# Performance work log

Measured on AMD Instinct MI355X. Metric: run time of the kernel, lower is better.

The kernel has to match this reference:

```python
import jax, jax.numpy as jnp
import numpy as np

B, N, DIM = 4, 1024, 768
H, GP = 12, 64
HD = DIM // H
SCALE = HD ** -0.5


def setup_inputs() -> dict:
    key = jax.random.key(0)
    ks = jax.random.split(key, 7)
    s = DIM ** -0.5
    return {
        "x": jax.random.normal(ks[0], (B, N, DIM), dtype=jnp.float32),
        "W_qkv": jax.random.normal(ks[1], (3 * DIM, DIM), dtype=jnp.float32) * s,
        "b_qkv": jnp.zeros((3 * DIM,), dtype=jnp.float32),
        "W_gp": jax.random.normal(ks[2], (GP, DIM), dtype=jnp.float32) * s,
        "alpha": jax.random.normal(ks[3], (1, H, 1, 1), dtype=jnp.float32),
        "W_proj": jax.random.normal(ks[4], (DIM, DIM), dtype=jnp.float32) * s,
        "b_proj": jnp.zeros((DIM,), dtype=jnp.float32),
    }


def reference(x, W_qkv, b_qkv, W_gp, alpha, W_proj, b_proj):
    b, n, c = x.shape
    # qkv projection, split into heads: [b, h, n, hd]
    qkv = x @ W_qkv.T + b_qkv
    q, k, v = jnp.split(qkv, 3, axis=-1)
    def to_heads(t):
        return t.reshape(b, n, H, HD).transpose(0, 2, 1, 3)
    q, k, v = to_heads(q), to_heads(k), to_heads(v)

    # raw attention scores [b, h, n, n]
    attn = jnp.einsum('bhnd,bhmd->bhnm', q, k) * SCALE

    # group similarity: gp weight viewed as [h, gp, hd]
    gp = W_gp.reshape(H, GP, HD)
    gw = jnp.einsum('bhnd,hmd->bhnm', v, gp)          # [b, h, n, gp]
    gw = jax.nn.gelu(gw, approximate=False)           # exact GELU (torch default)
    gw = jax.nn.softmax(gw, axis=-1)
    G = jnp.einsum('bhnm,bhkm->bhnk', gw, gw)         # [b, h, n, n]

    # gated combination
    attn = jax.nn.softmax(attn * G, axis=-1)
    a = jax.nn.sigmoid(alpha)                          # [1, h, 1, 1]
    A = (1.0 - a) * attn + a * G
    # column-sum renormalization (sum over query dim 2)
    A = A / (A.sum(axis=2, keepdims=True) + 1e-8)

    out = jnp.einsum('bhnm,bhmd->bhnd', A, v)
    out = out.transpose(0, 2, 1, 3).reshape(b, n, c)
    return out @ W_proj.T + b_proj
```

## Files before the change

kernel.cpp:

```cpp
#include <hip/hip_runtime.h>
#include <math.h>

namespace {

constexpr int kN   = 1024;
constexpr int kDim = 768;
constexpr int kH   = 12;
constexpr int kBH  = 48;
constexpr float kScale = 0.125f;

typedef __attribute__((ext_vector_type(8))) short short8;
typedef __attribute__((ext_vector_type(4))) short short4v;
typedef __attribute__((ext_vector_type(4))) float f32x4;
typedef __attribute__((ext_vector_type(16))) float f32x16;
typedef __attribute__((ext_vector_type(4))) uint uint4v;

#define MFMA(a, b, c)   __builtin_amdgcn_mfma_f32_16x16x32_bf16(a, b, c, 0, 0, 0)
#define MFMA32(a, b, c) __builtin_amdgcn_mfma_f32_32x32x16_bf16(a, b, c, 0, 0, 0)

__device__ __forceinline__ ushort f2bf(float f) {
  uint u = __builtin_bit_cast(uint, f);
  u += 0x7fffu + ((u >> 16) & 1u);
  return (ushort)(u >> 16);
}
__device__ __forceinline__ float bf2f(ushort h) {
  uint u = ((uint)h) << 16;
  return __builtin_bit_cast(float, u);
}
__device__ __forceinline__ void split8(const float* f, short8& hi, short8& lo) {
  #pragma unroll
  for (int i = 0; i < 8; i++) {
    const ushort h = f2bf(f[i]);
    hi[i] = (short)h;
    lo[i] = (short)f2bf(f[i] - bf2f(h));
  }
}
__device__ __forceinline__ uint packbf(float a, float b) {
  return (uint)f2bf(a) | ((uint)f2bf(b) << 16);
}

__device__ __forceinline__ void gl16(const short* g, short* l) {
  __builtin_amdgcn_global_load_lds(
      (const __attribute__((address_space(1))) void*)g,
      (__attribute__((address_space(3))) void*)l, 16, 0, 0);
}

__device__ __forceinline__ short8 frag(const short* t, int row, int chunk) {
  return *(const short8*)(t + row * 64 + ((chunk ^ (row & 7)) << 3));
}

template<int ROWS, int W>
__device__ __forceinline__ void stage_tile(short* dst, const short* src,
                                           int stride, int w, int l) {
  #pragma unroll
  for (int c = 0; c < ROWS / 8; c += W) {
    const int cc = c + w;
    const int row0 = cc << 3;
    const int row = row0 + (l >> 3);
    const int ch = (l & 7) ^ (row & 7);
    gl16(src + (size_t)row * stride + (ch << 3), dst + row0 * 64);
  }
}

__global__ __launch_bounds__(256) void k_split(const float* __restrict__ src,
                                               short* __restrict__ h,
                                               short* __restrict__ l) {
  const size_t i = ((size_t)blockIdx.x * 256 + threadIdx.x) * 4;
  const float4 f = *(const float4*)(src + i);
  const float ff[4] = {f.x, f.y, f.z, f.w};
  short4v hv, lv;
  #pragma unroll
  for (int j = 0; j < 4; j++) {
    const ushort u = f2bf(ff[j]);
    hv[j] = (short)u;
    lv[j] = (short)f2bf(ff[j] - bf2f(u));
  }
  *(short4v*)(h + i) = hv;
  *(short4v*)(l + i) = lv;
}

__global__ __launch_bounds__(512) void k_qkv(const short* __restrict__ xh,
                                             const short* __restrict__ xl,
                                             const short* __restrict__ wh,
                                             const short* __restrict__ wl,
                                             const float* __restrict__ bias,
                                             short* __restrict__ qh, short* __restrict__ ql,
                                             short* __restrict__ kh, short* __restrict__ kl,
                                             short* __restrict__ vh, short* __restrict__ vl) {
  __shared__ __align__(16) short sb[2][32768];
  const int bx = blockIdx.x, by = blockIdx.y;
  const int tid = threadIdx.x, w = tid >> 6, lane = tid & 63;
  const int wr = w >> 2, wc = w & 3;
  const short* Asrc_h = xh + (size_t)(by * 128) * kDim;
  const short* Asrc_l = xl + (size_t)(by * 128) * kDim;
  const short* Bsrc_h = wh + (size_t)(bx * 128) * kDim;
  const short* Bsrc_l = wl + (size_t)(bx * 128) * kDim;

  f32x4 acc[4][2] = {};
  {
    short* nb = sb[0];
    stage_tile<128, 8>(nb,          Asrc_h, kDim, w, lane);
    stage_tile<128, 8>(nb + 8192,   Asrc_l, kDim, w, lane);
    stage_tile<128, 8>(nb + 16384,  Bsrc_h, kDim, w, lane);
    stage_tile<128, 8>(nb + 24576,  Bsrc_l, kDim, w, lane);
  }
  int p = 0;
  #pragma unroll 1
  for (int t = 0; t < 12; ++t) {
    __syncthreads();
    if (t < 11) {
      const int k0 = (t + 1) * 64;
      short* nb = sb[p ^ 1];
      stage_tile<128, 8>(nb,         Asrc_h + k0, kDim, w, lane);
      stage_tile<128, 8>(nb + 8192,  Asrc_l + k0, kDim, w, lane);
      stage_tile<128, 8>(nb + 16384, Bsrc_h + k0, kDim, w, lane);
      stage_tile<128, 8>(nb + 24576, Bsrc_l + k0, kDim, w, lane);
    }
    const short* cb = sb[p];
    #pragma unroll
    for (int s = 0; s < 2; ++s) {
      const int ch = (s << 2) + (lane >> 4);
      short8 af[4], alf[4], bf_[2], blf[2];
      #pragma unroll
      for (int i = 0; i < 4; i++) {
        const int ar = wr * 64 + i * 16 + (lane & 15);
        af[i]  = frag(cb, ar, ch);
        alf[i] = frag(cb + 8192, ar, ch);
      }
      #pragma unroll
      for (int j = 0; j < 2; j++) {
        const int br = wc * 32 + j * 16 + (lane & 15);
        bf_[j] = frag(cb + 16384, br, ch);
        blf[j] = frag(cb + 24576, br, ch);
      }
      #pragma unroll
      for (int i = 0; i < 4; i++)
        #pragma unroll
        for (int j = 0; j < 2; j++) {
          acc[i][j] = MFMA(af[i], bf_[j], acc[i][j]);
          acc[i][j] = MFMA(af[i], blf[j], acc[i][j]);
          acc[i][j] = MFMA(alf[i], bf_[j], acc[i][j]);
        }
    }
    p ^= 1;
  }
  #pragma unroll
  for (int j = 0; j < 2; j++) {
    const int col = bx * 128 + wc * 32 + j * 16 + (lane & 15);
    const int part = col / 768;
    const int rem = col - part * 768;
    const int hh = rem >> 6, d = rem & 63;
    short* dh = (part == 0) ? qh : ((part == 1) ? kh : vh);
    short* dl = (part == 0) ? ql : ((part == 1) ? kl : vl);
    const float bv = bias[col];
    #pragma unroll
    for (int i = 0; i < 4; i++) {
      #pragma unroll
      for (int r = 0; r < 4; r++) {
        const int gr = by * 128 + wr * 64 + i * 16 + ((lane >> 4) << 2) + r;
        const int b = gr >> 10, n = gr & 1023;
        const float val = acc[i][j][r] + bv;
        const ushort hu = f2bf(val);
        const size_t idx = (size_t)((b * kH + hh) * kN + n) * 64 + d;
        dh[idx] = (short)hu;
        dl[idx] = (short)f2bf(val - bf2f(hu));
      }
    }
  }
}

__global__ __launch_bounds__(512) void k_gw(const short* __restrict__ vh,
                                            const short* __restrict__ vl,
                                            const float* __restrict__ Wgp,
                                            short* __restrict__ gwh,
                                            short* __restrict__ gwl) {
  const int bh = blockIdx.x;
  const int h = bh % kH;
  const int n0 = blockIdx.y << 7;
  const int tid = threadIdx.x, w = tid >> 6, lane = tid & 63;
  __shared__ __align__(16) short gph[4096], gpl[4096];
  {
    const int r = tid >> 3, c = tid & 7;
    float f[8] __attribute__((aligned(16)));
    *(float4*)(f + 0) = *(const float4*)(Wgp + h * 4096 + r * 64 + c * 8);
    *(float4*)(f + 4) = *(const float4*)(Wgp + h * 4096 + r * 64 + c * 8 + 4);
    short8 hh, ll;
    split8(f, hh, ll);
    const int slot = c ^ (r & 7);
    *(short8*)(gph + r * 64 + slot * 8) = hh;
    *(short8*)(gpl + r * 64 + slot * 8) = ll;
  }
  short8 vhf[2], vlf[2];
  const size_t arow = (size_t)(bh * kN + n0 + w * 16 + (lane & 15)) * 64 + ((lane >> 4) << 3);
  vhf[0] = *(const short8*)(vh + arow); vhf[1] = *(const short8*)(vh + arow + 32);
  vlf[0] = *(const short8*)(vl + arow); vlf[1] = *(const short8*)(vl + arow + 32);
  __syncthreads();

  f32x4 aU[4] = {};
  #pragma unroll
  for (int msub = 0; msub < 4; msub++) {
    #pragma unroll
    for (int s = 0; s < 2; s++) {
      const int row = (msub << 4) + (lane & 15);
      const int ch = (s << 2) + (lane >> 4);
      const short8 bh_ = frag(gph, row, ch);
      const short8 bl_ = frag(gpl, row, ch);
      aU[msub] = MFMA(vhf[s], bh_, aU[msub]);
      aU[msub] = MFMA(vhf[s], bl_, aU[msub]);
      aU[msub] = MFMA(vlf[s], bh_, aU[msub]);
    }
  }
  #pragma unroll
  for (int r = 0; r < 4; r++) {
    float u[4];
    #pragma unroll
    for (int m = 0; m < 4; m++) {
      const float a = aU[m][r];
      u[m] = 0.5f * a * (1.0f + erff(a * 0.70710678118654752f));
    }
    float mx = fmaxf(fmaxf(u[0], u[1]), fmaxf(u[2], u[3]));
    #pragma unroll
    for (int msk = 1; msk < 16; msk <<= 1) mx = fmaxf(mx, __shfl_xor(mx, msk));
    float e[4], ssum = 0.f;
    #pragma unroll
    for (int m = 0; m < 4; m++) { e[m] = __expf(u[m] - mx); ssum += e[m]; }
    #pragma unroll
    for (int msk = 1; msk < 16; msk <<= 1) ssum += __shfl_xor(ssum, msk);
    const float inv = 1.0f / ssum;
    const int n = n0 + w * 16 + ((lane >> 4) << 2) + r;
    #pragma unroll
    for (int m = 0; m < 4; m++) {
      const float g = e[m] * inv;
      const ushort hu = f2bf(g);
      const size_t idx = (size_t)(bh * kN + n) * 64 + (m << 4) + (lane & 15);
      gwh[idx] = (short)hu;
      gwl[idx] = (short)f2bf(g - bf2f(hu));
    }
  }
}

__global__ __launch_bounds__(256) void k_vt(const short* __restrict__ vh,
                                            const float* __restrict__ rcolv,
                                            short* __restrict__ vtg) {
  const int bh = blockIdx.x;
  const int n0 = blockIdx.y << 6;
  __shared__ short t[64][80];
  const int tid = threadIdx.x;
  {
    const int n = tid >> 2, d0 = (tid & 3) << 4;
    const float rc = rcolv[bh * kN + n0 + n];
    const short8 a = *(const short8*)(vh + (size_t)(bh * kN + n0 + n) * 64 + d0);
    const short8 b = *(const short8*)(vh + (size_t)(bh * kN + n0 + n) * 64 + d0 + 8);
    #pragma unroll
    for (int i = 0; i < 8; ++i) {
      t[d0 + i][n]     = (short)f2bf(bf2f((ushort)a[i]) * rc);
      t[d0 + 8 + i][n] = (short)f2bf(bf2f((ushort)b[i]) * rc);
    }
  }
  __syncthreads();
  const int d = tid >> 2, j0 = (tid & 3) << 4;
  short* dst = vtg + (size_t)bh * 65536 + (size_t)d * 1024 + n0 + j0;
  *(short8*)(dst)     = *(const short8*)(&t[d][j0]);
  *(short8*)(dst + 8) = *(const short8*)(&t[d][j0 + 8]);
}

__global__ __launch_bounds__(256) void k_denom(const short* __restrict__ qh,
                                               const short* __restrict__ ql,
                                               const short* __restrict__ kh,
                                               const short* __restrict__ kl,
                                               const short* __restrict__ gwh,
                                               const short* __restrict__ gwl,
                                               float* __restrict__ rdenom) {
  const int bh = blockIdx.x;
  const int n0 = blockIdx.y << 7;
  const int tid = threadIdx.x, w = tid >> 6, lane = tid & 63;
  const int lc = lane & 31, hl = lane >> 5;
  __shared__ __align__(16) short sb[16384];

  short8 qB[4], qlB[4], gB[4], glB[4];
  {
    const size_t nrow = (size_t)(bh * kN + n0 + w * 32 + lc) * 64;
    #pragma unroll
    for (int ks = 0; ks < 4; ks++) {
      const int off = ks * 16 + (hl << 3);
      qB[ks]  = *(const short8*)(qh  + nrow + off);
      qlB[ks] = *(const short8*)(ql  + nrow + off);
      gB[ks]  = *(const short8*)(gwh + nrow + off);
      glB[ks] = *(const short8*)(gwl + nrow + off);
    }
  }
  float dsum = 0.f;
  #pragma unroll 1
  for (int t = 0; t < 16; ++t) {
    __syncthreads();
    const size_t mo = (size_t)(bh * kN + t * 64) * 64;
    stage_tile<64, 4>(sb,         kh  + mo, 64, w, lane);
    stage_tile<64, 4>(sb + 4096,  kl  + mo, 64, w, lane);
    stage_tile<64, 4>(sb + 8192,  gwh + mo, 64, w, lane);
    stage_tile<64, 4>(sb + 12288, gwl + mo, 64, w, lane);
    __syncthreads();
    #pragma unroll
    for (int at = 0; at < 2; ++at) {
      f32x16 aS = {}, aG = {};
      #pragma unroll
      for (int ks = 0; ks < 4; ++ks) {
        const int row = at * 32 + lc;
        const int ck = ks * 2 + hl;
        const short8 Ah_ = frag(sb, row, ck);
        const short8 Al_ = frag(sb + 4096, row, ck);
        const short8 Eh_ = frag(sb + 8192, row, ck);
        const short8 El_ = frag(sb + 12288, row, ck);
        aS = MFMA32(Ah_, qB[ks], aS);
        aS = MFMA32(Al_, qB[ks], aS);
        aS = MFMA32(Ah_, qlB[ks], aS);
        aG = MFMA32(Eh_, gB[ks], aG);
        aG = MFMA32(El_, gB[ks], aG);
        aG = MFMA32(Eh_, glB[ks], aG);
      }
      #pragma unroll
      for (int r = 0; r < 16; ++r)
        dsum += __expf(aS[r] * kScale * aG[r]);
    }
  }
  dsum += __shfl_xor(dsum, 32);
  if (lane < 32) rdenom[bh * kN + n0 + w * 32 + lane] = 1.0f / dsum;
}

__global__ __launch_bounds__(256) void k_colsum(const short* __restrict__ qh,
                                                const short* __restrict__ ql,
                                                const short* __restrict__ kh,
                                                const short* __restrict__ kl,
                                                const short* __restrict__ gwh,
                                                const short* __restrict__ gwl,
                                                const float* __restrict__ rdenom,
                                                const float* __restrict__ alpha,
                                                float* __restrict__ rcolv) {
  const int bh = blockIdx.x;
  const int m0 = blockIdx.y << 7;
  const int tid = threadIdx.x, w = tid >> 6, lane = tid & 63;
  const int lc = lane & 31, hl = lane >> 5;
  __shared__ __align__(16) short sb[16384];
  __shared__ float rdl[64];
  const float ah_ = 1.0f / (1.0f + __expf(-alpha[bh % kH]));
  const float om = 1.0f - ah_;

  short8 kB[4], klB[4], gB[4], glB[4];
  {
    const size_t mrow = (size_t)(bh * kN + m0 + w * 32 + lc) * 64;
    #pragma unroll
    for (int ks = 0; ks < 4; ks++) {
      const int off = ks * 16 + (hl << 3);
      kB[ks]  = *(const short8*)(kh  + mrow + off);
      klB[ks] = *(const short8*)(kl  + mrow + off);
      gB[ks]  = *(const short8*)(gwh + mrow + off);
      glB[ks] = *(const short8*)(gwl + mrow + off);
    }
  }
  float csum = 0.f;
  #pragma unroll 1
  for (int t = 0; t < 16; ++t) {
    __syncthreads();
    const size_t no = (size_t)(bh * kN + t * 64) * 64;
    stage_tile<64, 4>(sb,         qh  + no, 64, w, lane);
    stage_tile<64, 4>(sb + 4096,  ql  + no, 64, w, lane);
    stage_tile<64, 4>(sb + 8192,  gwh + no, 64, w, lane);
    stage_tile<64, 4>(sb + 12288, gwl + no, 64, w, lane);
    if (tid < 64) rdl[tid] = rdenom[bh * kN + t * 64 + tid];
    __syncthreads();
    #pragma unroll
    for (int at = 0; at < 2; ++at) {
      f32x16 aS = {}, aG = {};
      #pragma unroll
      for (int ks = 0; ks < 4; ++ks) {
        const int row = at * 32 + lc;
        const int ck = ks * 2 + hl;
        const short8 Ah_ = frag(sb, row, ck);
        const short8 Al_ = frag(sb + 4096, row, ck);
        const short8 Eh_ = frag(sb + 8192, row, ck);
        const short8 El_ = frag(sb + 12288, row, ck);
        aS = MFMA32(Ah_, kB[ks], aS);
        aS = MFMA32(Al_, kB[ks], aS);
        aS = MFMA32(Ah_, klB[ks], aS);
        aG = MFMA32(Eh_, gB[ks], aG);
        aG = MFMA32(El_, gB[ks], aG);
        aG = MFMA32(Eh_, glB[ks], aG);
      }
      #pragma unroll
      for (int r = 0; r < 16; ++r) {
        const int nr = at * 32 + (r & 3) + ((r >> 2) << 3) + (hl << 2);
        const float g = aG[r];
        csum += om * (__expf(aS[r] * kScale * g) * rdl[nr]) + ah_ * g;
      }
    }
  }
  csum += __shfl_xor(csum, 32);
  if (lane < 32) rcolv[bh * kN + m0 + w * 32 + lane] = 1.0f / (csum + 1e-8f);
}

__global__ __launch_bounds__(256) void k_out(const short* __restrict__ qh,
                                             const short* __restrict__ ql,
                                             const short* __restrict__ kh,
                                             const short* __restrict__ kl,
                                             const short* __restrict__ vtg,
                                             const short* __restrict__ gwh,
                                             const short* __restrict__ gwl,
                                             const float* __restrict__ rdenom,
                                             const float* __restrict__ alpha,
                                             short* __restrict__ ctxh,
                                             short* __restrict__ ctxl) {
  const int bh = blockIdx.x;
  const int h = bh % kH;
  const int b = bh / kH;
  const int n0 = blockIdx.y << 7;
  const int tid = threadIdx.x, w = tid >> 6, lane = tid & 63;
  const int lc = lane & 31, hl = lane >> 5;
  __shared__ __align__(16) short sb[20480];
  const float ah_ = 1.0f / (1.0f + __expf(-alpha[h]));
  const float om = 1.0f - ah_;

  short8 qB[4], qlB[4], gB[4], glB[4];
  {
    const size_t nrow = (size_t)(bh * kN + n0 + w * 32 + lc) * 64;
    #pragma unroll
    for (int ks = 0; ks < 4; ks++) {
      const int off = ks * 16 + (hl << 3);
      qB[ks]  = *(const short8*)(qh  + nrow + off);
      qlB[ks] = *(const short8*)(ql  + nrow + off);
      gB[ks]  = *(const short8*)(gwh + nrow + off);
      glB[ks] = *(const short8*)(gwl + nrow + off);
    }
  }
  const float rdn = rdenom[bh * kN + n0 + w * 32 + lc];
  f32x16 oac[2] = {};

  #pragma unroll 1
  for (int t = 0; t < 16; ++t) {
    __syncthreads();
    const size_t mo = (size_t)(bh * kN + t * 64) * 64;
    stage_tile<64, 4>(sb,         kh  + mo, 64, w, lane);
    stage_tile<64, 4>(sb + 4096,  kl  + mo, 64, w, lane);
    stage_tile<64, 4>(sb + 8192,  gwh + mo, 64, w, lane);
    stage_tile<64, 4>(sb + 12288, gwl + mo, 64, w, lane);
    stage_tile<64, 4>(sb + 16384, vtg + (size_t)bh * 65536 + t * 64, kN, w, lane);
    __syncthreads();
    short8 pf[4];
    #pragma unroll
    for (int at = 0; at < 2; ++at) {
      f32x16 aS = {}, aG = {};
      #pragma unroll
      for (int ks = 0; ks < 4; ++ks) {
        const int row = at * 32 + lc;
        const int ck = ks * 2 + hl;
        const short8 Ah_ = frag(sb, row, ck);
        const short8 Al_ = frag(sb + 4096, row, ck);
        const short8 Eh_ = frag(sb + 8192, row, ck);
        const short8 El_ = frag(sb + 12288, row, ck);
        aS = MFMA32(Ah_, qB[ks], aS);
        aS = MFMA32(Al_, qB[ks], aS);
        aS = MFMA32(Ah_, qlB[ks], aS);
        aG = MFMA32(Eh_, gB[ks], aG);
        aG = MFMA32(El_, gB[ks], aG);
        aG = MFMA32(Eh_, glB[ks], aG);
      }
      float a[16];
      #pragma unroll
      for (int r = 0; r < 16; ++r) {
        const float g = aG[r];
        const float p = __expf(aS[r] * kScale * g) * rdn;
        a[r] = om * p + ah_ * g;
      }
      uint W[8], Ws[8];
      #pragma unroll
      for (int j = 0; j < 8; ++j) W[j] = packbf(a[2 * j], a[2 * j + 1]);
      #pragma unroll
      for (int j = 0; j < 8; ++j) Ws[j] = __shfl_xor(W[j], 32);
      {
        uint4v b0, b1;
        b0[0] = hl ? Ws[2] : W[0];  b0[1] = hl ? Ws[3] : W[1];
        b0[2] = hl ? W[2]  : Ws[0]; b0[3] = hl ? W[3]  : Ws[1];
        b1[0] = hl ? Ws[6] : W[4];  b1[1] = hl ? Ws[7] : W[5];
        b1[2] = hl ? W[6]  : Ws[4]; b1[3] = hl ? W[7]  : Ws[5];
        pf[at * 2 + 0] = __builtin_bit_cast(short8, b0);
        pf[at * 2 + 1] = __builtin_bit_cast(short8, b1);
      }
    }
    #pragma unroll
    for (int dt = 0; dt < 2; ++dt)
      #pragma unroll
      for (int ks = 0; ks < 4; ++ks) {
        const short8 va = frag(sb + 16384, dt * 32 + lc, ks * 2 + hl);
        oac[dt] = MFMA32(va, pf[ks], oac[dt]);
      }
  }
  __syncthreads();
  float* ow = (float*)sb;
  const int wbase = w * 32 * 68;
  #pragma unroll
  for (int dt = 0; dt < 2; ++dt)
    #pragma unroll
    for (int r = 0; r < 16; ++r) {
      const int d = dt * 32 + (r & 3) + ((r >> 2) << 3) + (hl << 2);
      ow[wbase + lc * 68 + d] = oac[dt][r];
    }
  __syncthreads();
  {
    const int rowi = tid >> 1;
    const int d0 = (tid & 1) << 5;
    const float* src = ow + (rowi >> 5) * 32 * 68 + (rowi & 31) * 68 + d0;
    float f[32] __attribute__((aligned(16)));
    #pragma unroll
    for (int j = 0; j < 8; ++j) *(float4*)(f + 4 * j) = *(const float4*)(src + 4 * j);
    const int n = n0 + rowi;
    short* dsth = ctxh + (size_t)(b * kN + n) * kDim + h * 64 + d0;
    short* dstl = ctxl + (size_t)(b * kN + n) * kDim + h * 64 + d0;
    #pragma unroll
    for (int g8 = 0; g8 < 4; ++g8) {
      short8 hi, lo;
      split8(f + 8 * g8, hi, lo);
      *(short8*)(dsth + 8 * g8) = hi;
      *(short8*)(dstl + 8 * g8) = lo;
    }
  }
}

__global__ __launch_bounds__(512) void k_proj(const short* __restrict__ ch_,
                                              const short* __restrict__ cl_,
                                              const short* __restrict__ wh,
                                              const short* __restrict__ wl,
                                              const float* __restrict__ bias,
                                              float* __restrict__ out) {
  __shared__ __align__(16) short sb[2][32768];
  const int bx = blockIdx.x, by = blockIdx.y;
  const int tid = threadIdx.x, w = tid >> 6, lane = tid & 63;
  const int wr = w >> 2, wc = w & 3;
  const short* Asrc_h = ch_ + (size_t)(by * 128) * kDim;
  const short* Asrc_l = cl_ + (size_t)(by * 128) * kDim;
  const short* Bsrc_h = wh + (size_t)(bx * 128) * kDim;
  const short* Bsrc_l = wl + (size_t)(bx * 128) * kDim;

  f32x4 acc[4][2] = {};
  {
    short* nb = sb[0];
    stage_tile<128, 8>(nb,         Asrc_h, kDim, w, lane);
    stage_tile<128, 8>(nb + 8192,  Asrc_l, kDim, w, lane);
    stage_tile<128, 8>(nb + 16384, Bsrc_h, kDim, w, lane);
    stage_tile<128, 8>(nb + 24576, Bsrc_l, kDim, w, lane);
  }
  int p = 0;
  #pragma unroll 1
  for (int t = 0; t < 12; ++t) {
    __syncthreads();
    if (t < 11) {
      const int k0 = (t + 1) * 64;
      short* nb = sb[p ^ 1];
      stage_tile<128, 8>(nb,         Asrc_h + k0, kDim, w, lane);
      stage_tile<128, 8>(nb + 8192,  Asrc_l + k0, kDim, w, lane);
      stage_tile<128, 8>(nb + 16384, Bsrc_h + k0, kDim, w, lane);
      stage_tile<128, 8>(nb + 24576, Bsrc_l + k0, kDim, w, lane);
    }
    const short* cb = sb[p];
    #pragma unroll
    for (int s = 0; s < 2; ++s) {
      const int ch = (s << 2) + (lane >> 4);
      short8 af[4], alf[4], bf_[2], blf[2];
      #pragma unroll
      for (int i = 0; i < 4; i++) {
        const int ar = wr * 64 + i * 16 + (lane & 15);
        af[i]  = frag(cb, ar, ch);
        alf[i] = frag(cb + 8192, ar, ch);
      }
      #pragma unroll
      for (int j = 0; j < 2; j++) {
        const int br = wc * 32 + j * 16 + (lane & 15);
        bf_[j] = frag(cb + 16384, br, ch);
        blf[j] = frag(cb + 24576, br, ch);
      }
      #pragma unroll
      for (int i = 0; i < 4; i++)
        #pragma unroll
        for (int j = 0; j < 2; j++) {
          acc[i][j] = MFMA(af[i], bf_[j], acc[i][j]);
          acc[i][j] = MFMA(af[i], blf[j], acc[i][j]);
          acc[i][j] = MFMA(alf[i], bf_[j], acc[i][j]);
          acc[i][j] = MFMA(alf[i], blf[j], acc[i][j]);
        }
    }
    p ^= 1;
  }
  #pragma unroll
  for (int j = 0; j < 2; j++) {
    const int col = bx * 128 + wc * 32 + j * 16 + (lane & 15);
    const float bv = bias[col];
    #pragma unroll
    for (int i = 0; i < 4; i++) {
      #pragma unroll
      for (int r = 0; r < 4; r++) {
        const int row = by * 128 + wr * 64 + i * 16 + ((lane >> 4) << 2) + r;
        out[(size_t)row * kDim + col] = acc[i][j][r] + bv;
      }
    }
  }
}

}

extern "C" void kernel_launch(void* const* d_in, const int* in_sizes, int n_in,
                              void* d_out, int out_size, void* d_ws, size_t ws_size,
                              hipStream_t stream) {
  const float* x     = (const float*)d_in[0];
  const float* Wqkv  = (const float*)d_in[1];
  const float* bqkv  = (const float*)d_in[2];
  const float* Wgp   = (const float*)d_in[3];
  const float* alpha = (const float*)d_in[4];
  const float* Wproj = (const float*)d_in[5];
  const float* bproj = (const float*)d_in[6];
  float* out = (float*)d_out;

  const size_t he = 3145728;
  short* qh  = (short*)d_ws;
  short* ql  = qh + he;
  short* kh  = ql + he;
  short* kl  = kh + he;
  short* vh  = kl + he;
  short* vl  = vh + he;
  short* gwh = vl + he;
  short* gwl = gwh + he;
  short* xh  = gwl + he;
  short* xl  = xh + he;
  float* rdenom = (float*)(xl + he);
  float* rcolv  = rdenom + (size_t)kBH * kN;

  short* Wqh = gwh;  short* Wql = gwl;
  short* vtg = vl;
  short* ctxh = xh;  short* ctxl = xl;
  short* Wph = qh;   short* Wpl = ql;

  k_split<<<3072, 256, 0, stream>>>(x, xh, xl);
  k_split<<<1728, 256, 0, stream>>>(Wqkv, Wqh, Wql);
  k_qkv  <<<dim3(18, 32), 512, 0, stream>>>(xh, xl, Wqh, Wql, bqkv,
                                            qh, ql, kh, kl, vh, vl);
  k_gw   <<<dim3(kBH, 8), 512, 0, stream>>>(vh, vl, Wgp, gwh, gwl);
  k_denom<<<dim3(kBH, 8), 256, 0, stream>>>(qh, ql, kh, kl, gwh, gwl, rdenom);
  k_colsum<<<dim3(kBH, 8), 256, 0, stream>>>(qh, ql, kh, kl, gwh, gwl,
                                             rdenom, alpha, rcolv);
  k_vt   <<<dim3(kBH, 16), 256, 0, stream>>>(vh, rcolv, vtg);
  k_out  <<<dim3(kBH, 8), 256, 0, stream>>>(qh, ql, kh, kl, vtg, gwh, gwl,
                                            rdenom, alpha, ctxh, ctxl);
  k_split<<<576, 256, 0, stream>>>(Wproj, Wph, Wpl);
  k_proj <<<dim3(6, 32), 512, 0, stream>>>(ctxh, ctxl, Wph, Wpl, bproj, out);
}
```

Baseline: 274.2 us.

## Split key dimension across wave groups in attention kernels and fold scale into q

```diff
diff --git a/kernel.cpp b/kernel.cpp
--- a/kernel.cpp
+++ b/kernel.cpp
@@ -153,13 +153,14 @@
     short* dh = (part == 0) ? qh : ((part == 1) ? kh : vh);
     short* dl = (part == 0) ? ql : ((part == 1) ? kl : vl);
     const float bv = bias[col];
+    const float scl = (part == 0) ? kScale : 1.0f;
     #pragma unroll
     for (int i = 0; i < 4; i++) {
       #pragma unroll
       for (int r = 0; r < 4; r++) {
         const int gr = by * 128 + wr * 64 + i * 16 + ((lane >> 4) << 2) + r;
         const int b = gr >> 10, n = gr & 1023;
-        const float val = acc[i][j][r] + bv;
+        const float val = (acc[i][j][r] + bv) * scl;
         const ushort hu = f2bf(val);
         const size_t idx = (size_t)((b * kH + hh) * kN + n) * 64 + d;
         dh[idx] = (short)hu;
@@ -264,22 +265,25 @@
   *(short8*)(dst + 8) = *(const short8*)(&t[d][j0 + 8]);
 }
 
-__global__ __launch_bounds__(256) void k_denom(const short* __restrict__ qh,
-                                               const short* __restrict__ ql,
-                                               const short* __restrict__ kh,
-                                               const short* __restrict__ kl,
-                                               const short* __restrict__ gwh,
-                                               const short* __restrict__ gwl,
-                                               float* __restrict__ rdenom) {
+__global__ __launch_bounds__(256, 3) void k_denom(const short* __restrict__ qh,
+                                                  const short* __restrict__ ql,
+                                                  const short* __restrict__ kh,
+                                                  const short* __restrict__ kl,
+                                                  const short* __restrict__ gwh,
+                                                  const short* __restrict__ gwl,
+                                                  float* __restrict__ rdenom) {
   const int bh = blockIdx.x;
-  const int n0 = blockIdx.y << 7;
+  const int n0 = blockIdx.y << 6;
   const int tid = threadIdx.x, w = tid >> 6, lane = tid & 63;
   const int lc = lane & 31, hl = lane >> 5;
-  __shared__ __align__(16) short sb[16384];
+  const int nw = w & 1, mh = w >> 1;
+  __shared__ __align__(16) short sb[32768];
+  __shared__ float part[4][32];
+  const short* my = sb + mh * 16384;
 
   short8 qB[4], qlB[4], gB[4], glB[4];
   {
-    const size_t nrow = (size_t)(bh * kN + n0 + w * 32 + lc) * 64;
+    const size_t nrow = (size_t)(bh * kN + n0 + nw * 32 + lc) * 64;
     #pragma unroll
     for (int ks = 0; ks < 4; ks++) {
       const int off = ks * 16 + (hl << 3);
@@ -291,13 +295,18 @@
   }
   float dsum = 0.f;
   #pragma unroll 1
-  for (int t = 0; t < 16; ++t) {
-    __syncthreads();
-    const size_t mo = (size_t)(bh * kN + t * 64) * 64;
-    stage_tile<64, 4>(sb,         kh  + mo, 64, w, lane);
-    stage_tile<64, 4>(sb + 4096,  kl  + mo, 64, w, lane);
-    stage_tile<64, 4>(sb + 8192,  gwh + mo, 64, w, lane);
-    stage_tile<64, 4>(sb + 12288, gwl + mo, 64, w, lane);
+  for (int t = 0; t < 8; ++t) {
+    __syncthreads();
+    const size_t mo0 = (size_t)(bh * kN + t * 64) * 64;
+    const size_t mo1 = (size_t)(bh * kN + 512 + t * 64) * 64;
+    stage_tile<64, 4>(sb,          kh  + mo0, 64, w, lane);
+    stage_tile<64, 4>(sb + 4096,   kl  + mo0, 64, w, lane);
+    stage_tile<64, 4>(sb + 8192,   gwh + mo0, 64, w, lane);
+    stage_tile<64, 4>(sb + 12288,  gwl + mo0, 64, w, lane);
+    stage_tile<64, 4>(sb + 16384,  kh  + mo1, 64, w, lane);
+    stage_tile<64, 4>(sb + 20480,  kl  + mo1, 64, w, lane);
+    stage_tile<64, 4>(sb + 24576,  gwh + mo1, 64, w, lane);
+    stage_tile<64, 4>(sb + 28672,  gwl + mo1, 64, w, lane);
     __syncthreads();
     #pragma unroll
     for (int at = 0; at < 2; ++at) {
@@ -306,10 +315,10 @@
       for (int ks = 0; ks < 4; ++ks) {
         const int row = at * 32 + lc;
         const int ck = ks * 2 + hl;
-        const short8 Ah_ = frag(sb, row, ck);
-        const short8 Al_ = frag(sb + 4096, row, ck);
-        const short8 Eh_ = frag(sb + 8192, row, ck);
-        const short8 El_ = frag(sb + 12288, row, ck);
+        const short8 Ah_ = frag(my, row, ck);
+        const short8 Al_ = frag(my + 4096, row, ck);
+        const short8 Eh_ = frag(my + 8192, row, ck);
+        const short8 El_ = frag(my + 12288, row, ck);
         aS = MFMA32(Ah_, qB[ks], aS);
         aS = MFMA32(Al_, qB[ks], aS);
         aS = MFMA32(Ah_, qlB[ks], aS);
@@ -319,34 +328,41 @@
       }
       #pragma unroll
       for (int r = 0; r < 16; ++r)
-        dsum += __expf(aS[r] * kScale * aG[r]);
+        dsum += __expf(aS[r] * aG[r]);
     }
   }
   dsum += __shfl_xor(dsum, 32);
-  if (lane < 32) rdenom[bh * kN + n0 + w * 32 + lane] = 1.0f / dsum;
-}
-
-__global__ __launch_bounds__(256) void k_colsum(const short* __restrict__ qh,
-                                                const short* __restrict__ ql,
-                                                const short* __restrict__ kh,
-                                                const short* __restrict__ kl,
-                                                const short* __restrict__ gwh,
-                                                const short* __restrict__ gwl,
-                                                const float* __restrict__ rdenom,
-                                                const float* __restrict__ alpha,
-                                                float* __restrict__ rcolv) {
+  if (hl == 0) part[w][lc] = dsum;
+  __syncthreads();
+  if (tid < 64)
+    rdenom[bh * kN + n0 + tid] =
+        1.0f / (part[tid >> 5][tid & 31] + part[2 + (tid >> 5)][tid & 31]);
+}
+
+__global__ __launch_bounds__(256, 3) void k_colsum(const short* __restrict__ qh,
+                                                   const short* __restrict__ ql,
+                                                   const short* __restrict__ kh,
+                                                   const short* __restrict__ kl,
+                                                   const short* __restrict__ gwh,
+                                                   const short* __restrict__ gwl,
+                                                   const float* __restrict__ rdenom,
+                                                   const float* __restrict__ alpha,
+                                                   float* __restrict__ rcolv) {
   const int bh = blockIdx.x;
-  const int m0 = blockIdx.y << 7;
+  const int m0 = blockIdx.y << 6;
   const int tid = threadIdx.x, w = tid >> 6, lane = tid & 63;
   const int lc = lane & 31, hl = lane >> 5;
-  __shared__ __align__(16) short sb[16384];
-  __shared__ float rdl[64];
+  const int mw = w & 1, nh = w >> 1;
+  __shared__ __align__(16) short sb[32768];
+  __shared__ float part[4][32];
+  __shared__ float rdl[2][64];
+  const short* my = sb + nh * 16384;
   const float ah_ = 1.0f / (1.0f + __expf(-alpha[bh % kH]));
   const float om = 1.0f - ah_;
 
   short8 kB[4], klB[4], gB[4], glB[4];
   {
-    const size_t mrow = (size_t)(bh * kN + m0 + w * 32 + lc) * 64;
+    const size_t mrow = (size_t)(bh * kN + m0 + mw * 32 + lc) * 64;
     #pragma unroll
     for (int ks = 0; ks < 4; ks++) {
       const int off = ks * 16 + (hl << 3);
@@ -358,14 +374,21 @@
   }
   float csum = 0.f;
   #pragma unroll 1
-  for (int t = 0; t < 16; ++t) {
-    __syncthreads();
-    const size_t no = (size_t)(bh * kN + t * 64) * 64;
-    stage_tile<64, 4>(sb,         qh  + no, 64, w, lane);
-    stage_tile<64, 4>(sb + 4096,  ql  + no, 64, w, lane);
-    stage_tile<64, 4>(sb + 8192,  gwh + no, 64, w, lane);
-    stage_tile<64, 4>(sb + 12288, gwl + no, 64, w, lane);
-    if (tid < 64) rdl[tid] = rdenom[bh * kN + t * 64 + tid];
+  for (int t = 0; t < 8; ++t) {
+    __syncthreads();
+    const size_t no0 = (size_t)(bh * kN + t * 64) * 64;
+    const size_t no1 = (size_t)(bh * kN + 512 + t * 64) * 64;
+    stage_tile<64, 4>(sb,          qh  + no0, 64, w, lane);
+    stage_tile<64, 4>(sb + 4096,   ql  + no0, 64, w, lane);
+    stage_tile<64, 4>(sb + 8192,   gwh + no0, 64, w, lane);
+    stage_tile<64, 4>(sb + 12288,  gwl + no0, 64, w, lane);
+    stage_tile<64, 4>(sb + 16384,  qh  + no1, 64, w, lane);
+    stage_tile<64, 4>(sb + 20480,  ql  + no1, 64, w, lane);
+    stage_tile<64, 4>(sb + 24576,  gwh + no1, 64, w, lane);
+    stage_tile<64, 4>(sb + 28672,  gwl + no1, 64, w, lane);
+    if (tid < 128)
+      rdl[tid >> 6][tid & 63] =
+          rdenom[bh * kN + (tid >> 6) * 512 + t * 64 + (tid & 63)];
     __syncthreads();
     #pragma unroll
     for (int at = 0; at < 2; ++at) {
@@ -374,10 +397,10 @@
       for (int ks = 0; ks < 4; ++ks) {
         const int row = at * 32 + lc;
         const int ck = ks * 2 + hl;
-        const short8 Ah_ = frag(sb, row, ck);
-        const short8 Al_ = frag(sb + 4096, row, ck);
-        const short8 Eh_ = frag(sb + 8192, row, ck);
-        const short8 El_ = frag(sb + 12288, row, ck);
+        const short8 Ah_ = frag(my, row, ck);
+        const short8 Al_ = frag(my + 4096, row, ck);
+        const short8 Eh_ = frag(my + 8192, row, ck);
+        const short8 El_ = frag(my + 12288, row, ck);
         aS = MFMA32(Ah_, kB[ks], aS);
         aS = MFMA32(Al_, kB[ks], aS);
         aS = MFMA32(Ah_, klB[ks], aS);
@@ -389,38 +412,44 @@
       for (int r = 0; r < 16; ++r) {
         const int nr = at * 32 + (r & 3) + ((r >> 2) << 3) + (hl << 2);
         const float g = aG[r];
-        csum += om * (__expf(aS[r] * kScale * g) * rdl[nr]) + ah_ * g;
+        csum += om * (__expf(aS[r] * g) * rdl[nh][nr]) + ah_ * g;
       }
     }
   }
   csum += __shfl_xor(csum, 32);
-  if (lane < 32) rcolv[bh * kN + m0 + w * 32 + lane] = 1.0f / (csum + 1e-8f);
-}
-
-__global__ __launch_bounds__(256) void k_out(const short* __restrict__ qh,
-                                             const short* __restrict__ ql,
-                                             const short* __restrict__ kh,
-                                             const short* __restrict__ kl,
-                                             const short* __restrict__ vtg,
-                                             const short* __restrict__ gwh,
-                                             const short* __restrict__ gwl,
-                                             const float* __restrict__ rdenom,
-                                             const float* __restrict__ alpha,
-                                             short* __restrict__ ctxh,
-                                             short* __restrict__ ctxl) {
+  if (hl == 0) part[w][lc] = csum;
+  __syncthreads();
+  if (tid < 64)
+    rcolv[bh * kN + m0 + tid] =
+        1.0f / (part[tid >> 5][tid & 31] + part[2 + (tid >> 5)][tid & 31] + 1e-8f);
+}
+
+__global__ __launch_bounds__(512, 4) void k_out(const short* __restrict__ qh,
+                                                const short* __restrict__ ql,
+                                                const short* __restrict__ kh,
+                                                const short* __restrict__ kl,
+                                                const short* __restrict__ vtg,
+                                                const short* __restrict__ gwh,
+                                                const short* __restrict__ gwl,
+                                                const float* __restrict__ rdenom,
+                                                const float* __restrict__ alpha,
+                                                short* __restrict__ ctxh,
+                                                short* __restrict__ ctxl) {
   const int bh = blockIdx.x;
   const int h = bh % kH;
   const int b = bh / kH;
   const int n0 = blockIdx.y << 7;
   const int tid = threadIdx.x, w = tid >> 6, lane = tid & 63;
   const int lc = lane & 31, hl = lane >> 5;
-  __shared__ __align__(16) short sb[20480];
+  const int nw = w & 3, mh = w >> 2;
+  __shared__ __align__(16) short sb[40960];
   const float ah_ = 1.0f / (1.0f + __expf(-alpha[h]));
   const float om = 1.0f - ah_;
+  const short* my = sb + mh * 20480;
 
   short8 qB[4], qlB[4], gB[4], glB[4];
   {
-    const size_t nrow = (size_t)(bh * kN + n0 + w * 32 + lc) * 64;
+    const size_t nrow = (size_t)(bh * kN + n0 + nw * 32 + lc) * 64;
     #pragma unroll
     for (int ks = 0; ks < 4; ks++) {
       const int off = ks * 16 + (hl << 3);
@@ -430,18 +459,24 @@
       glB[ks] = *(const short8*)(gwl + nrow + off);
     }
   }
-  const float rdn = rdenom[bh * kN + n0 + w * 32 + lc];
+  const float rdn = rdenom[bh * kN + n0 + nw * 32 + lc];
   f32x16 oac[2] = {};
 
   #pragma unroll 1
-  for (int t = 0; t < 16; ++t) {
-    __syncthreads();
-    const size_t mo = (size_t)(bh * kN + t * 64) * 64;
-    stage_tile<64, 4>(sb,         kh  + mo, 64, w, lane);
-    stage_tile<64, 4>(sb + 4096,  kl  + mo, 64, w, lane);
-    stage_tile<64, 4>(sb + 8192,  gwh + mo, 64, w, lane);
-    stage_tile<64, 4>(sb + 12288, gwl + mo, 64, w, lane);
-    stage_tile<64, 4>(sb + 16384, vtg + (size_t)bh * 65536 + t * 64, kN, w, lane);
+  for (int t = 0; t < 8; ++t) {
+    __syncthreads();
+    const size_t mo0 = (size_t)(bh * kN + t * 64) * 64;
+    const size_t mo1 = (size_t)(bh * kN + 512 + t * 64) * 64;
+    stage_tile<64, 8>(sb,          kh  + mo0, 64, w, lane);
+    stage_tile<64, 8>(sb + 4096,   kl  + mo0, 64, w, lane);
+    stage_tile<64, 8>(sb + 8192,   gwh + mo0, 64, w, lane);
+    stage_tile<64, 8>(sb + 12288,  gwl + mo0, 64, w, lane);
+    stage_tile<64, 8>(sb + 16384,  vtg + (size_t)bh * 65536 + t * 64, kN, w, lane);
+    stage_tile<64, 8>(sb + 20480,  kh  + mo1, 64, w, lane);
+    stage_tile<64, 8>(sb + 24576,  kl  + mo1, 64, w, lane);
+    stage_tile<64, 8>(sb + 28672,  gwh + mo1, 64, w, lane);
+    stage_tile<64, 8>(sb + 32768,  gwl + mo1, 64, w, lane);
+    stage_tile<64, 8>(sb + 36864,  vtg + (size_t)bh * 65536 + 512 + t * 64, kN, w, lane);
     __syncthreads();
     short8 pf[4];
     #pragma unroll
@@ -451,10 +486,10 @@
       for (int ks = 0; ks < 4; ++ks) {
         const int row = at * 32 + lc;
         const int ck = ks * 2 + hl;
-        const short8 Ah_ = frag(sb, row, ck);
-        const short8 Al_ = frag(sb + 4096, row, ck);
-        const short8 Eh_ = frag(sb + 8192, row, ck);
-        const short8 El_ = frag(sb + 12288, row, ck);
+        const short8 Ah_ = frag(my, row, ck);
+        const short8 Al_ = frag(my + 4096, row, ck);
+        const short8 Eh_ = frag(my + 8192, row, ck);
+        const short8 El_ = frag(my + 12288, row, ck);
         aS = MFMA32(Ah_, qB[ks], aS);
         aS = MFMA32(Al_, qB[ks], aS);
         aS = MFMA32(Ah_, qlB[ks], aS);
@@ -466,7 +501,7 @@
       #pragma unroll
       for (int r = 0; r < 16; ++r) {
         const float g = aG[r];
-        const float p = __expf(aS[r] * kScale * g) * rdn;
+        const float p = __expf(aS[r] * g) * rdn;
         a[r] = om * p + ah_ * g;
       }
       uint W[8], Ws[8];
@@ -488,33 +523,45 @@
     for (int dt = 0; dt < 2; ++dt)
       #pragma unroll
       for (int ks = 0; ks < 4; ++ks) {
-        const short8 va = frag(sb + 16384, dt * 32 + lc, ks * 2 + hl);
+        const short8 va = frag(my + 16384, dt * 32 + lc, ks * 2 + hl);
         oac[dt] = MFMA32(va, pf[ks], oac[dt]);
       }
   }
   __syncthreads();
-  float* ow = (float*)sb;
-  const int wbase = w * 32 * 68;
-  #pragma unroll
-  for (int dt = 0; dt < 2; ++dt)
-    #pragma unroll
-    for (int r = 0; r < 16; ++r) {
-      const int d = dt * 32 + (r & 3) + ((r >> 2) << 3) + (hl << 2);
-      ow[wbase + lc * 68 + d] = oac[dt][r];
-    }
+  float* buf = (float*)sb;
+  if (mh == 1) {
+    #pragma unroll
+    for (int dt = 0; dt < 2; ++dt)
+      #pragma unroll
+      for (int r = 0; r < 16; ++r) {
+        const int d = dt * 32 + (r & 3) + ((r >> 2) << 3) + (hl << 2);
+        buf[(nw * 32 + lc) * 68 + d] = oac[dt][r];
+      }
+  }
   __syncthreads();
-  {
-    const int rowi = tid >> 1;
-    const int d0 = (tid & 1) << 5;
-    const float* src = ow + (rowi >> 5) * 32 * 68 + (rowi & 31) * 68 + d0;
-    float f[32] __attribute__((aligned(16)));
-    #pragma unroll
-    for (int j = 0; j < 8; ++j) *(float4*)(f + 4 * j) = *(const float4*)(src + 4 * j);
+  if (mh == 0) {
+    #pragma unroll
+    for (int dt = 0; dt < 2; ++dt)
+      #pragma unroll
+      for (int r = 0; r < 16; ++r) {
+        const int d = dt * 32 + (r & 3) + ((r >> 2) << 3) + (hl << 2);
+        const int idx = (nw * 32 + lc) * 68 + d;
+        buf[idx] = oac[dt][r] + buf[idx];
+      }
+  }
+  __syncthreads();
+  {
+    const int rowi = tid >> 2;
+    const int d0 = (tid & 3) << 4;
+    float f[16] __attribute__((aligned(16)));
+    #pragma unroll
+    for (int j = 0; j < 4; ++j)
+      *(float4*)(f + 4 * j) = *(const float4*)(&buf[rowi * 68 + d0 + 4 * j]);
     const int n = n0 + rowi;
     short* dsth = ctxh + (size_t)(b * kN + n) * kDim + h * 64 + d0;
     short* dstl = ctxl + (size_t)(b * kN + n) * kDim + h * 64 + d0;
     #pragma unroll
-    for (int g8 = 0; g8 < 4; ++g8) {
+    for (int g8 = 0; g8 < 2; ++g8) {
       short8 hi, lo;
       split8(f + 8 * g8, hi, lo);
       *(short8*)(dsth + 8 * g8) = hi;
@@ -640,11 +687,11 @@
   k_qkv  <<<dim3(18, 32), 512, 0, stream>>>(xh, xl, Wqh, Wql, bqkv,
                                             qh, ql, kh, kl, vh, vl);
   k_gw   <<<dim3(kBH, 8), 512, 0, stream>>>(vh, vl, Wgp, gwh, gwl);
-  k_denom<<<dim3(kBH, 8), 256, 0, stream>>>(qh, ql, kh, kl, gwh, gwl, rdenom);
-  k_colsum<<<dim3(kBH, 8), 256, 0, stream>>>(qh, ql, kh, kl, gwh, gwl,
-                                             rdenom, alpha, rcolv);
+  k_denom<<<dim3(kBH, 16), 256, 0, stream>>>(qh, ql, kh, kl, gwh, gwl, rdenom);
+  k_colsum<<<dim3(kBH, 16), 256, 0, stream>>>(qh, ql, kh, kl, gwh, gwl,
+                                              rdenom, alpha, rcolv);
   k_vt   <<<dim3(kBH, 16), 256, 0, stream>>>(vh, rcolv, vtg);
-  k_out  <<<dim3(kBH, 8), 256, 0, stream>>>(qh, ql, kh, kl, vtg, gwh, gwl,
+  k_out  <<<dim3(kBH, 8), 512, 0, stream>>>(qh, ql, kh, kl, vtg, gwh, gwl,
                                             rdenom, alpha, ctxh, ctxl);
   k_split<<<576, 256, 0, stream>>>(Wproj, Wph, Wpl);
   k_proj <<<dim3(6, 32), 512, 0, stream>>>(ctxh, ctxl, Wph, Wpl, bproj, out);
```

After: 348.1 us. 1.27x slower.
